# Kernel optimization log

Measured on AMD Instinct MI355X. Metric: run time of the kernel, lower is better.

The kernel has to match this reference:

```python
import jax, jax.numpy as jnp
import numpy as np

HIDDEN = 512
NHEADS = 8
ALPHA = 0.1
NUM_HOP = 4
MASK_VAL = -16384.0
LN_EPS = 1e-5


def setup_inputs() -> dict:
    key = jax.random.key(0)
    ks = jax.random.split(key, 10)
    B, N, H = 8, 1024, HIDDEN
    s = 1.0 / np.sqrt(H)
    x = jax.random.normal(ks[0], (B, N, H), dtype=jnp.float32)
    adj = jax.random.randint(ks[1], (B, N, N), 0, 2, dtype=jnp.int32)
    Wq = jax.random.uniform(ks[2], (H, H), jnp.float32, -s, s)
    bq = jax.random.uniform(ks[3], (H,), jnp.float32, -s, s)
    Wk = jax.random.uniform(ks[4], (H, H), jnp.float32, -s, s)
    bk = jax.random.uniform(ks[5], (H,), jnp.float32, -s, s)
    Wv = jax.random.uniform(ks[6], (H, H), jnp.float32, -s, s)
    bv = jax.random.uniform(ks[7], (H,), jnp.float32, -s, s)
    gamma = jnp.ones((H,), jnp.float32)
    beta = jnp.zeros((H,), jnp.float32)
    return {"x": x, "adj": adj, "Wq": Wq, "bq": bq, "Wk": Wk, "bk": bk,
            "Wv": Wv, "bv": bv, "gamma": gamma, "beta": beta}


def reference(x, adj, Wq, bq, Wk, bk, Wv, bv, gamma, beta):
    B, N, H = x.shape
    u = H // NHEADS
    # torch Linear: y = x @ W^T + b
    q = x @ Wq.T + bq  # [B,N,H]
    k = x @ Wk.T + bk
    v = x @ Wv.T + bv
    # split hidden into contiguous head chunks (matches per-head slicing)
    qh = q.reshape(B, N, NHEADS, u).transpose(0, 2, 1, 3)  # [B,Hd,N,u]
    kh = k.reshape(B, N, NHEADS, u).transpose(0, 2, 1, 3)
    vh = v.reshape(B, N, NHEADS, u).transpose(0, 2, 1, 3)
    scores = jnp.einsum('bhnd,bhmd->bhnm', qh, kh)  # [B,Hd,N,N]
    mask = (adj == 0)[:, None, :, :]  # broadcast over heads
    scores = jnp.where(mask, MASK_VAL, scores)
    pros = jax.nn.softmax(scores, axis=-1)
    z_init = vh
    z = z_init
    for _ in range(NUM_HOP):
        z = (1.0 - ALPHA) * jnp.einsum('bhnm,bhmd->bhnd', pros, z) + ALPHA * z_init
    h_prime = z.transpose(0, 2, 1, 3).reshape(B, N, H)  # concat heads
    y = x + h_prime
    mu = jnp.mean(y, axis=-1, keepdims=True)
    var = jnp.mean((y - mu) ** 2, axis=-1, keepdims=True)
    return (y - mu) / jnp.sqrt(var + LN_EPS) * gamma + beta
```

## Files before the change

kernel.cpp:

```cpp
#include <hip/hip_runtime.h>
#include <hip/hip_bf16.h>

#define BB 8
#define NN 1024
#define HH 512
#define NHEADS 8
#define UU 64

typedef __attribute__((ext_vector_type(8))) short short8;
typedef __attribute__((ext_vector_type(4))) float f32x4;
typedef __attribute__((ext_vector_type(16))) float f32x16;
typedef unsigned short u16;
typedef unsigned char u8;

__device__ inline float b2f(unsigned short u) {
    union { float f; unsigned int i; } c; c.i = ((unsigned int)u) << 16; return c.f;
}
__device__ inline unsigned short f2b(float f) {
    __hip_bfloat16 h = __float2bfloat16(f);
    return *reinterpret_cast<unsigned short*>(&h);
}
__device__ inline unsigned int pkbf(float a, float b) {
    unsigned int r;
    asm("v_cvt_pk_bf16_f32 %0, %1, %2" : "=v"(r) : "v"(a), "v"(b));
    return r;
}
__device__ inline float upk_lo(unsigned int u) {
    union { float f; unsigned int i; } c; c.i = u << 16; return c.f;
}
__device__ inline float upk_hi(unsigned int u) {
    union { float f; unsigned int i; } c; c.i = u & 0xffff0000u; return c.f;
}
__device__ inline void gl_lds16(const void* g, void* l) {
    __builtin_amdgcn_global_load_lds(
        (const __attribute__((address_space(1))) unsigned int*)g,
        (__attribute__((address_space(3))) unsigned int*)l, 16, 0, 0);
}

__global__ __launch_bounds__(256) void prep(
    const float* __restrict__ x, const float* __restrict__ Wq,
    const float* __restrict__ Wk, const float* __restrict__ Wv,
    const int* __restrict__ adj,
    u16* __restrict__ xb, u16* __restrict__ Wb,
    unsigned int* __restrict__ adjpT)
{
    const int gid = blockIdx.x;
    if (gid < 2432) {
        const float* src;
        u16* dst;
        int base;
        if (gid < 2048) {
            src = x; dst = xb;
            base = (gid * 256 + threadIdx.x) * 8;
        } else {
            const int g = gid - 2048;
            const int which = g >> 7;
            const int slice = g & 127;
            src = which == 0 ? Wq : (which == 1 ? Wk : Wv);
            dst = Wb + (size_t)which * HH * HH;
            base = (slice * 256 + threadIdx.x) * 8;
        }
        const float4* sp = (const float4*)&src[base];
        float4 a = sp[0], b = sp[1];
        short8 o;
        o[0] = (short)f2b(a.x); o[1] = (short)f2b(a.y);
        o[2] = (short)f2b(a.z); o[3] = (short)f2b(a.w);
        o[4] = (short)f2b(b.x); o[5] = (short)f2b(b.y);
        o[6] = (short)f2b(b.z); o[7] = (short)f2b(b.w);
        *(short8*)&dst[base] = o;
    } else {
        const int wave = threadIdx.x >> 6, lane = threadIdx.x & 63;
        const int row = (gid - 2432) * 4 + wave;
        const int b = row >> 10, r = row & 1023;
        const int* ar = adj + (size_t)row * NN;
        unsigned int* ob = adjpT + (((size_t)b) << 15) + r;
        #pragma unroll
        for (int it = 0; it < 16; ++it) {
            int a = ar[it * 64 + lane];
            unsigned long long m = __ballot(a != 0);
            if (lane == 0) {
                ob[(size_t)(2 * it)     << 10] = (unsigned int)m;
                ob[(size_t)(2 * it + 1) << 10] = (unsigned int)(m >> 32);
            }
        }
    }
}

__global__ __launch_bounds__(256, 4) void qkv_gemm(
    const u16* __restrict__ xb, const u16* __restrict__ Wb,
    const float* __restrict__ bq, const float* __restrict__ bk,
    const float* __restrict__ bv,
    u16* __restrict__ q, u16* __restrict__ k, u16* __restrict__ v,
    u8* __restrict__ v8t)
{
    const int which = blockIdx.z;
    const u16* W      = Wb + (size_t)which * HH * HH;
    const float* bias = which == 0 ? bq : (which == 1 ? bk : bv);
    u16* out          = which == 0 ? q  : (which == 1 ? k  : v);

    const int tid = threadIdx.x;
    const int wave = tid >> 6, lane = tid & 63;
    const int ln = lane & 15, quad = lane >> 4;
    const int wr = (wave >> 1) * 64, wc = (wave & 1) * 64;
    const int rowbase = blockIdx.x * 128, colbase = blockIdx.y * 128;

    __shared__ __align__(16) char smem[128 * 136 * 2];
    u16* Cs = (u16*)smem;

    f32x4 acc[4][4];
    #pragma unroll
    for (int ri = 0; ri < 4; ++ri)
        #pragma unroll
        for (int ci = 0; ci < 4; ++ci) acc[ri][ci] = (f32x4){0.f, 0.f, 0.f, 0.f};

    const int lr = lane >> 2;
    const int sg = lane & 3;

    auto STAGE = [&](int buf, int kk) {
        char* Ab = smem + buf * 16384;
        char* Bb = smem + 8192 + buf * 16384;
        #pragma unroll
        for (int i = 0; i < 2; ++i) {
            int r = wave * 32 + i * 16 + lr;
            gl_lds16(&xb[(size_t)(rowbase + r) * HH + kk + sg * 8],
                     Ab + (wave * 32 + i * 16) * 64);
            gl_lds16(&W[(size_t)(colbase + r) * HH + kk + sg * 8],
                     Bb + (wave * 32 + i * 16) * 64);
        }
    };

    STAGE(0, 0);
    for (int s = 0; s < 16; ++s) {
        __syncthreads();
        if (s < 15) STAGE((s + 1) & 1, (s + 1) * 32);
        const u16* As = (const u16*)(smem + (s & 1) * 16384);
        const u16* Bs = (const u16*)(smem + 8192 + (s & 1) * 16384);

        short8 bfr[4];
        #pragma unroll
        for (int ci = 0; ci < 4; ++ci)
            bfr[ci] = *(const short8*)&Bs[(wc + ci * 16 + ln) * 32 + quad * 8];
        #pragma unroll
        for (int ri = 0; ri < 4; ++ri) {
            short8 af = *(const short8*)&As[(wr + ri * 16 + ln) * 32 + quad * 8];
            #pragma unroll
            for (int ci = 0; ci < 4; ++ci)
                acc[ri][ci] = __builtin_amdgcn_mfma_f32_16x16x32_bf16(af, bfr[ci], acc[ri][ci], 0, 0, 0);
        }
    }

    __syncthreads();
    #pragma unroll
    for (int ci = 0; ci < 4; ++ci) {
        int col = wc + ci * 16 + ln;
        float bb = bias[colbase + col];
        #pragma unroll
        for (int ri = 0; ri < 4; ++ri) {
            #pragma unroll
            for (int r = 0; r < 4; ++r) {
                int row = wr + ri * 16 + quad * 4 + r;
                Cs[row * 136 + col] = f2b(acc[ri][ci][r] + bb);
            }
        }
    }
    __syncthreads();
    {
        int row = tid >> 1, half = tid & 1;
        int gcol0 = colbase + half * 64;
        int hh = gcol0 >> 6;
        int grow = rowbase + row;
        int bidx = grow >> 10, n = grow & 1023;
        u16* op = &out[(((size_t)(bidx * NHEADS + hh)) * NN + n) * UU];
        const u16* cp = &Cs[row * 136 + half * 64];
        #pragma unroll
        for (int j = 0; j < 8; ++j)
            *(short8*)(op + j * 8) = *(const short8*)(cp + j * 8);
    }
    if (which == 2) {
        const int d_local = tid >> 1, nh = tid & 1;
        const int hloc = d_local >> 6, d = d_local & 63;
        const int bidx = rowbase >> 10, n0 = (rowbase & 1023) + nh * 64;
        const int bh = bidx * NHEADS + (colbase >> 6) + hloc;
        u8* vp = v8t + ((size_t)bh << 16) + (size_t)d * 1024 + n0;
        #pragma unroll
        for (int j = 0; j < 16; ++j) {
            const u16* cp = &Cs[(nh * 64 + j * 4) * 136 + d_local];
            float f0 = b2f(cp[0]);
            float f1 = b2f(cp[136]);
            float f2 = b2f(cp[272]);
            float f3 = b2f(cp[408]);
            int lo = __builtin_amdgcn_cvt_pk_fp8_f32(f0, f1, 0, false);
            unsigned int dw = (unsigned int)__builtin_amdgcn_cvt_pk_fp8_f32(f2, f3, lo, true);
            *(unsigned int*)(vp + j * 4) = dw;
        }
    }
}

__global__ __launch_bounds__(512, 4) void scores_softmax(
    const u16* __restrict__ q, const u16* __restrict__ kmat,
    const unsigned int* __restrict__ adjpT, u8* __restrict__ P8)
{
    const int gid = blockIdx.x;
    const int j = gid >> 3;
    const int h = gid & 7;
    const int b = j >> 5;
    const int bx = j & 31;
    const int bh = b * NHEADS + h;

    const int tid = threadIdx.x;
    const int kq = tid >> 6, lane = tid & 63;
    const int l31 = lane & 31, hi = lane >> 5;
    const int n = bx * 32 + l31;
    const int kt0 = kq * 4;

    __shared__ float rs[8][32];

    short8 qf[4];
    const u16* qp = &q[((size_t)bh * NN + n) * UU + hi * 8];
    #pragma unroll
    for (int f = 0; f < 4; ++f) qf[f] = *(const short8*)(qp + f * 16);

    const u16* kbase = kmat + (size_t)bh * NN * UU + (size_t)(kt0 * 32 + l31) * UU + hi * 8;
    const unsigned int* mbase = adjpT + (((size_t)b) << 15) + n;

    unsigned int mv[4];
    #pragma unroll
    for (int i = 0; i < 4; ++i)
        mv[i] = mbase[(size_t)(kt0 + i) << 10] >> (4 * hi);

    const float L2E = 1.442695041f;
    const float C0 = -46.16624f;
    const float CM = -100000.0f;

    unsigned int eb[4][4][2];
    float rs0 = 0.f, rs1 = 0.f, rs2 = 0.f, rs3 = 0.f;

    short8 kf[4];
    #pragma unroll
    for (int f = 0; f < 4; ++f) kf[f] = *(const short8*)(kbase + f * 16);

    #pragma unroll
    for (int i = 0; i < 4; ++i) {
        f32x16 acc;
        #pragma unroll
        for (int jj = 0; jj < 16; ++jj) acc[jj] = 0.f;
        #pragma unroll
        for (int f = 0; f < 4; ++f)
            acc = __builtin_amdgcn_mfma_f32_32x32x16_bf16(kf[f], qf[f], acc, 0, 0, 0);
        if (i < 3) {
            const u16* kn = kbase + (size_t)(i + 1) * (32 * UU);
            #pragma unroll
            for (int f = 0; f < 4; ++f) kf[f] = *(const short8*)(kn + f * 16);
        }
        const unsigned int m2 = mv[i];
        #pragma unroll
        for (int g = 0; g < 4; ++g) {
            float e[4];
            #pragma unroll
            for (int r = 0; r < 4; ++r) {
                const int koff = r + 8 * g;
                float addv = ((m2 >> koff) & 1u) ? C0 : CM;
                e[r] = __builtin_amdgcn_exp2f(fmaf(L2E, acc[g * 4 + r], addv));
            }
            if (g == 0) rs0 += (e[0] + e[1]) + (e[2] + e[3]);
            else if (g == 1) rs1 += (e[0] + e[1]) + (e[2] + e[3]);
            else if (g == 2) rs2 += (e[0] + e[1]) + (e[2] + e[3]);
            else rs3 += (e[0] + e[1]) + (e[2] + e[3]);
            eb[i][g][0] = pkbf(e[0], e[1]);
            eb[i][g][1] = pkbf(e[2], e[3]);
        }
    }
    float rsum = (rs0 + rs1) + (rs2 + rs3);
    rsum += __shfl_xor(rsum, 32);
    if (lane < 32) rs[kq][lane] = rsum;
    __syncthreads();
    const float total = ((rs[0][l31] + rs[1][l31]) + (rs[2][l31] + rs[3][l31]))
                      + ((rs[4][l31] + rs[5][l31]) + (rs[6][l31] + rs[7][l31]));
    const float scl = 16.0f / total;

    u8* pb = P8 + (((size_t)bh) << 20) + (size_t)(n >> 4) * 16384
           + (n & 15) * 32 + hi * 16;
    #pragma unroll
    for (int i = 0; i < 4; ++i) {
        unsigned int dw[4];
        #pragma unroll
        for (int g = 0; g < 4; ++g) {
            float e0 = upk_lo(eb[i][g][0]) * scl;
            float e1 = upk_hi(eb[i][g][0]) * scl;
            float e2 = upk_lo(eb[i][g][1]) * scl;
            float e3 = upk_hi(eb[i][g][1]) * scl;
            int lo = __builtin_amdgcn_cvt_pk_fp8_f32(e0, e1, 0, false);
            dw[g] = (unsigned int)__builtin_amdgcn_cvt_pk_fp8_f32(e2, e3, lo, true);
        }
        unsigned int sendA = hi ? dw[0] : dw[2];
        unsigned int sendB = hi ? dw[1] : dw[3];
        unsigned int recvA = (unsigned int)__shfl_xor((int)sendA, 32);
        unsigned int recvB = (unsigned int)__shfl_xor((int)sendB, 32);
        uint4 o;
        o.x = hi ? recvA : dw[0];
        o.y = hi ? dw[2] : recvA;
        o.z = hi ? recvB : dw[1];
        o.w = hi ? dw[3] : recvB;
        *(uint4*)(pb + (size_t)(kt0 + i) * 512) = o;
    }
}

__global__ __launch_bounds__(512) void hop(
    const u8* __restrict__ P8, const u8* __restrict__ z8in,
    const u16* __restrict__ v, u8* __restrict__ z8out,
    u16* __restrict__ zbf_out, int last)
{
    const int b = blockIdx.z, h = blockIdx.y, rt = blockIdx.x;
    const int bh = b * NHEADS + h;
    const int tid = threadIdx.x;
    const int wave = tid >> 6, lane = tid & 63;
    const int ln = lane & 15, quad = lane >> 4;
    const int wrow = rt * 128 + wave * 16;

    __shared__ __align__(16) u8 zt[64 * 1040];

    const u8* zg = z8in + ((size_t)bh << 16);
    #pragma unroll
    for (int i = 0; i < 8; ++i) {
        int c = wave * 8 + i;
        gl_lds16(zg + (size_t)c * 1024 + lane * 16, (char*)zt + c * 1040);
    }

    const u8* pt = P8 + ((size_t)bh << 20) + (size_t)(rt * 8 + wave) * 16384
                 + ln * 32 + quad * 8;
    long pa[4];
    #pragma unroll
    for (int i = 0; i < 4; ++i) pa[i] = *(const long*)(pt + i * 512);

    __syncthreads();

    f32x4 acc[4];
    #pragma unroll
    for (int ci = 0; ci < 4; ++ci) acc[ci] = (f32x4){0.f, 0.f, 0.f, 0.f};

    #pragma unroll
    for (int kc = 0; kc < 32; ++kc) {
        long a = pa[kc & 3];
        if (kc + 4 < 32) pa[kc & 3] = *(const long*)(pt + (kc + 4) * 512);
        int kk = kc * 32;
        #pragma unroll
        for (int ci = 0; ci < 4; ++ci) {
            long bz = *(const long*)&zt[(ci * 16 + ln) * 1040 + kk + quad * 8];
            acc[ci] = __builtin_amdgcn_mfma_f32_16x16x32_fp8_fp8(a, bz, acc[ci], 0, 0, 0);
        }
    }

    if (last) {
        #pragma unroll
        for (int ci = 0; ci < 4; ++ci) {
            int col = ci * 16 + ln;
            #pragma unroll
            for (int r = 0; r < 4; ++r) {
                int row = wrow + quad * 4 + r;
                float vv = b2f(v[((size_t)bh * NN + row) * UU + col]);
                zbf_out[((size_t)(b * NN + row)) * HH + h * UU + col]
                    = f2b(0.05625f * acc[ci][r] + 0.1f * vv);
            }
        }
    } else {
        u8* zo = z8out + ((size_t)bh << 16);
        #pragma unroll
        for (int ci = 0; ci < 4; ++ci) {
            int col = ci * 16 + ln;
            float zv[4];
            #pragma unroll
            for (int r = 0; r < 4; ++r) {
                int row = wrow + quad * 4 + r;
                float vv = b2f(v[((size_t)bh * NN + row) * UU + col]);
                zv[r] = 0.05625f * acc[ci][r] + 0.1f * vv;
            }
            int lo = __builtin_amdgcn_cvt_pk_fp8_f32(zv[0], zv[1], 0, false);
            unsigned int dw = (unsigned int)__builtin_amdgcn_cvt_pk_fp8_f32(zv[2], zv[3], lo, true);
            *(unsigned int*)&zo[(size_t)col * 1024 + wrow + quad * 4] = dw;
        }
    }
}

__global__ __launch_bounds__(256) void resid_ln(
    const float* __restrict__ x, const u16* __restrict__ z,
    const float* __restrict__ gamma, const float* __restrict__ beta,
    float* __restrict__ out)
{
    const int r = blockIdx.x * 4 + (threadIdx.x >> 6);
    const int lane = threadIdx.x & 63;
    const size_t base = (size_t)r * HH + lane * 8;

    const float4* xp = (const float4*)&x[base];
    float4 x0 = xp[0], x1 = xp[1];
    short8 zv = *(const short8*)&z[base];
    float y[8];
    y[0] = x0.x + b2f((u16)zv[0]); y[1] = x0.y + b2f((u16)zv[1]);
    y[2] = x0.z + b2f((u16)zv[2]); y[3] = x0.w + b2f((u16)zv[3]);
    y[4] = x1.x + b2f((u16)zv[4]); y[5] = x1.y + b2f((u16)zv[5]);
    y[6] = x1.z + b2f((u16)zv[6]); y[7] = x1.w + b2f((u16)zv[7]);

    float s = 0.f, sq = 0.f;
    #pragma unroll
    for (int j = 0; j < 8; ++j) { s += y[j]; sq += y[j] * y[j]; }
    #pragma unroll
    for (int off = 32; off >= 1; off >>= 1) {
        s  += __shfl_xor(s, off);
        sq += __shfl_xor(sq, off);
    }
    const float mu = s * (1.0f / HH);
    const float var = sq * (1.0f / HH) - mu * mu;
    const float rstd = rsqrtf(var + 1e-5f);

    const float4* gp = (const float4*)&gamma[lane * 8];
    const float4* bp = (const float4*)&beta[lane * 8];
    float4 g0 = gp[0], g1 = gp[1], b0 = bp[0], b1 = bp[1];

    float4 o0, o1;
    o0.x = (y[0] - mu) * rstd * g0.x + b0.x;
    o0.y = (y[1] - mu) * rstd * g0.y + b0.y;
    o0.z = (y[2] - mu) * rstd * g0.z + b0.z;
    o0.w = (y[3] - mu) * rstd * g0.w + b0.w;
    o1.x = (y[4] - mu) * rstd * g1.x + b1.x;
    o1.y = (y[5] - mu) * rstd * g1.y + b1.y;
    o1.z = (y[6] - mu) * rstd * g1.z + b1.z;
    o1.w = (y[7] - mu) * rstd * g1.w + b1.w;
    float4* op = (float4*)&out[base];
    op[0] = o0; op[1] = o1;
}

extern "C" void kernel_launch(void* const* d_in, const int* in_sizes, int n_in,
                              void* d_out, int out_size, void* d_ws, size_t ws_size,
                              hipStream_t stream)
{
    const float* x   = (const float*)d_in[0];
    const int* adj   = (const int*)d_in[1];
    const float* Wq  = (const float*)d_in[2];
    const float* bq  = (const float*)d_in[3];
    const float* Wk  = (const float*)d_in[4];
    const float* bk  = (const float*)d_in[5];
    const float* Wv  = (const float*)d_in[6];
    const float* bv  = (const float*)d_in[7];
    const float* gamma = (const float*)d_in[8];
    const float* beta  = (const float*)d_in[9];
    float* out = (float*)d_out;

    const size_t E = (size_t)BB * NN * HH;
    u16* ws16 = (u16*)d_ws;
    u16* xb = ws16;
    u16* q  = ws16 + E;
    u16* k  = ws16 + 2 * E;
    u16* v  = ws16 + 3 * E;
    u16* za = ws16 + 4 * E;
    u16* Wb = ws16 + 5 * E;
    u8* base8 = (u8*)(ws16 + 5 * E + 786432);
    u8* P8  = base8;
    u8* z8a = base8 + ((size_t)64 << 20);
    u8* z8b = z8a + ((size_t)4 << 20);
    u8* v8t = z8b + ((size_t)4 << 20);
    unsigned int* adjpT = (unsigned int*)(v8t + ((size_t)4 << 20));

    prep<<<dim3(4480), 256, 0, stream>>>(x, Wq, Wk, Wv, adj, xb, Wb, adjpT);
    qkv_gemm<<<dim3(64, 4, 3), 256, 0, stream>>>(xb, Wb, bq, bk, bv, q, k, v, v8t);
    scores_softmax<<<dim3(2048), 512, 0, stream>>>(q, k, adjpT, P8);
    hop<<<dim3(8, NHEADS, BB), 512, 0, stream>>>(P8, v8t, v, z8a, za, 0);
    hop<<<dim3(8, NHEADS, BB), 512, 0, stream>>>(P8, z8a, v, z8b, za, 0);
    hop<<<dim3(8, NHEADS, BB), 512, 0, stream>>>(P8, z8b, v, z8a, za, 0);
    hop<<<dim3(8, NHEADS, BB), 512, 0, stream>>>(P8, z8a, v, z8b, za, 1);
    resid_ln<<<dim3(2048), 256, 0, stream>>>(x, za, gamma, beta, out);
}
```

Baseline: 261.8 us.

## Fuse four hop launches into one cooperative kernel keeping P in registers

Replaces the four separate `hop` launches with a single cooperative kernel, `hop4`. It loads each wave's fp8 attention-probability tile into registers once and keeps it there for all four propagation steps. Between steps it uses grid-wide syncs and writes z through the ping-pong global buffers. The aim is to avoid re-reading the 64 MB P8 matrix from memory on every hop and to remove three kernel launches. In exchange it pays for grid syncs and faces higher register pressure under `launch_bounds(512,4)`, which could cause spills. It falls back to the old four launches if the cooperative launch fails.

```diff
diff --git a/kernel.cpp b/kernel.cpp
--- a/kernel.cpp
+++ b/kernel.cpp
@@ -1,5 +1,8 @@
 #include <hip/hip_runtime.h>
 #include <hip/hip_bf16.h>
+#include <hip/hip_cooperative_groups.h>
+
+namespace cg = cooperative_groups;
 
 #define BB 8
 #define NN 1024
@@ -305,6 +308,98 @@
     }
 }
 
+__global__ __launch_bounds__(512, 4) void hop4(
+    const u8* __restrict__ P8, const u8* __restrict__ v8t,
+    const u16* __restrict__ v, u8* __restrict__ z8a, u8* __restrict__ z8b,
+    u16* __restrict__ zbf_out)
+{
+    const int b = blockIdx.z, h = blockIdx.y, rt = blockIdx.x;
+    const int bh = b * NHEADS + h;
+    const int tid = threadIdx.x;
+    const int wave = tid >> 6, lane = tid & 63;
+    const int ln = lane & 15, quad = lane >> 4;
+    const int wrow = rt * 128 + wave * 16;
+
+    __shared__ __align__(16) u8 zt[64 * 1040];
+
+    const u8* zg0 = v8t + ((size_t)bh << 16);
+    #pragma unroll
+    for (int i = 0; i < 8; ++i) {
+        int c = wave * 8 + i;
+        gl_lds16(zg0 + (size_t)c * 1024 + lane * 16, (char*)zt + c * 1040);
+    }
+
+    const u8* pt = P8 + ((size_t)bh << 20) + (size_t)(rt * 8 + wave) * 16384
+                 + ln * 32 + quad * 8;
+    long P[32];
+    #pragma unroll
+    for (int kc = 0; kc < 32; ++kc) P[kc] = *(const long*)(pt + kc * 512);
+
+    cg::grid_group grid = cg::this_grid();
+
+    __syncthreads();
+
+    const u8* srcs1to3[3] = { z8a, z8b, z8a };
+    u8* dsts[3] = { z8a, z8b, z8a };
+
+    #pragma unroll 1
+    for (int iter = 0; iter < 4; ++iter) {
+        f32x4 acc[4];
+        #pragma unroll
+        for (int ci = 0; ci < 4; ++ci) acc[ci] = (f32x4){0.f, 0.f, 0.f, 0.f};
+
+        #pragma unroll
+        for (int kc = 0; kc < 32; ++kc) {
+            int kk = kc * 32;
+            #pragma unroll
+            for (int ci = 0; ci < 4; ++ci) {
+                long bz = *(const long*)&zt[(ci * 16 + ln) * 1040 + kk + quad * 8];
+                acc[ci] = __builtin_amdgcn_mfma_f32_16x16x32_fp8_fp8(P[kc], bz, acc[ci], 0, 0, 0);
+            }
+        }
+
+        if (iter == 3) {
+            #pragma unroll
+            for (int ci = 0; ci < 4; ++ci) {
+                int col = ci * 16 + ln;
+                #pragma unroll
+                for (int r = 0; r < 4; ++r) {
+                    int row = wrow + quad * 4 + r;
+                    float vv = b2f(v[((size_t)bh * NN + row) * UU + col]);
+                    zbf_out[((size_t)(b * NN + row)) * HH + h * UU + col]
+                        = f2b(0.05625f * acc[ci][r] + 0.1f * vv);
+                }
+            }
+        } else {
+            u8* zo = dsts[iter] + ((size_t)bh << 16);
+            #pragma unroll
+            for (int ci = 0; ci < 4; ++ci) {
+                int col = ci * 16 + ln;
+                float zv[4];
+                #pragma unroll
+                for (int r = 0; r < 4; ++r) {
+                    int row = wrow + quad * 4 + r;
+                    float vv = b2f(v[((size_t)bh * NN + row) * UU + col]);
+                    zv[r] = 0.05625f * acc[ci][r] + 0.1f * vv;
+                }
+                int lo = __builtin_amdgcn_cvt_pk_fp8_f32(zv[0], zv[1], 0, false);
+                unsigned int dw = (unsigned int)__builtin_amdgcn_cvt_pk_fp8_f32(zv[2], zv[3], lo, true);
+                *(unsigned int*)&zo[(size_t)col * 1024 + wrow + quad * 4] = dw;
+            }
+            __threadfence();
+            grid.sync();
+            __threadfence();
+            const u8* zsrc = srcs1to3[iter] + ((size_t)bh << 16);
+            #pragma unroll
+            for (int i = 0; i < 8; ++i) {
+                int c = wave * 8 + i;
+                gl_lds16(zsrc + (size_t)c * 1024 + lane * 16, (char*)zt + c * 1040);
+            }
+            __syncthreads();
+        }
+    }
+}
+
 __global__ __launch_bounds__(512) void hop(
     const u8* __restrict__ P8, const u8* __restrict__ z8in,
     const u16* __restrict__ v, u8* __restrict__ z8out,
@@ -462,9 +557,19 @@
     prep<<<dim3(4480), 256, 0, stream>>>(x, Wq, Wk, Wv, adj, xb, Wb, adjpT);
     qkv_gemm<<<dim3(64, 4, 3), 256, 0, stream>>>(xb, Wb, bq, bk, bv, q, k, v, v8t);
     scores_softmax<<<dim3(2048), 512, 0, stream>>>(q, k, adjpT, P8);
-    hop<<<dim3(8, NHEADS, BB), 512, 0, stream>>>(P8, v8t, v, z8a, za, 0);
-    hop<<<dim3(8, NHEADS, BB), 512, 0, stream>>>(P8, z8a, v, z8b, za, 0);
-    hop<<<dim3(8, NHEADS, BB), 512, 0, stream>>>(P8, z8b, v, z8a, za, 0);
-    hop<<<dim3(8, NHEADS, BB), 512, 0, stream>>>(P8, z8a, v, z8b, za, 1);
+
+    {
+        void* args[] = { (void*)&P8, (void*)&v8t, (void*)&v,
+                         (void*)&z8a, (void*)&z8b, (void*)&za };
+        hipError_t ce = hipLaunchCooperativeKernel(
+            (const void*)hop4, dim3(8, NHEADS, BB), dim3(512), args, 0, stream);
+        if (ce != hipSuccess) {
+            hop<<<dim3(8, NHEADS, BB), 512, 0, stream>>>(P8, v8t, v, z8a, za, 0);
+            hop<<<dim3(8, NHEADS, BB), 512, 0, stream>>>(P8, z8a, v, z8b, za, 0);
+            hop<<<dim3(8, NHEADS, BB), 512, 0, stream>>>(P8, z8b, v, z8a, za, 0);
+            hop<<<dim3(8, NHEADS, BB), 512, 0, stream>>>(P8, z8a, v, z8b, za, 1);
+        }
+    }
+
     resid_ln<<<dim3(2048), 256, 0, stream>>>(x, za, gamma, beta, out);
 }
```

After: 993.5 us. +279.5%, slower.
